# Performance work log

Hardware: AMD Instinct MI355X
Metric: run time of the kernel (lower is better)

## Reference

```python
import jax, jax.numpy as jnp
import numpy as np

B, T, IN, H = 4096, 128, 768, 256


def setup_inputs() -> dict:
    key = jax.random.key(0)
    ks = jax.random.split(key, 5)
    s1 = 1.0 / np.sqrt(IN)
    s2 = 1.0 / np.sqrt(H)
    return {
        "x": jax.random.normal(ks[0], (B, IN), jnp.float32),
        "W1": jax.random.normal(ks[1], (T, IN, H), jnp.float32) * s1,
        "b1": jnp.zeros((T, H), jnp.float32),
        "W2": jax.random.normal(ks[2], (T, H, H), jnp.float32) * s2,
        "b2": jnp.zeros((T, H), jnp.float32),
        "W3": jax.random.normal(ks[3], (T, H), jnp.float32) * s2,
        "b3": jnp.zeros((T,), jnp.float32),
    }


def reference(x, W1, b1, W2, b2, W3, b3):
    # Per-task 3-layer MLP, vectorized over tasks. Dropout is eval-mode (identity).
    h = jax.nn.relu(jnp.einsum('bi,tih->bth', x, W1) + b1)          # [B, T, H]
    h = jax.nn.relu(jnp.einsum('bth,thk->btk', h, W2) + b2)         # [B, T, H]
    out = jnp.einsum('bth,th->bt', h, W3) + b3                      # [B, T]
    return out
```

## Files before the change

### kernel.cpp

```cpp
#include <hip/hip_runtime.h>
#include <cstdint>
#include <cstddef>

#define B_   4096
#define T_   128
#define IN_  768
#define H_   256
#define BM_  128
#define KC1  (IN_ / 32)
#define NS1  48
#define NS2  16

typedef __bf16 bf16_t;
typedef bf16_t bf16x8 __attribute__((ext_vector_type(8)));
typedef bf16_t bf16x4 __attribute__((ext_vector_type(4)));
typedef float  floatx16 __attribute__((ext_vector_type(16)));

#define MFMA32(a, b, c) __builtin_amdgcn_mfma_f32_32x32x16_bf16((a), (b), (c), 0, 0, 0)

__device__ __forceinline__ void lgkm0_barrier() {
    asm volatile("s_waitcnt lgkmcnt(0)" ::: "memory");
    __builtin_amdgcn_s_barrier();
    asm volatile("" ::: "memory");
}

__global__ __launch_bounds__(256)
void tile_all(const float* __restrict__ x, const float* __restrict__ W1,
              const float* __restrict__ W2, bf16_t* __restrict__ xt,
              bf16_t* __restrict__ w1t, bf16_t* __restrict__ w2t) {
    const int b   = blockIdx.x;
    const int tid = threadIdx.x;
    if (b < T_ * KC1 + T_ * 8) {
        const float* src; bf16_t* dst; int t, kc, K, KC;
        if (b < T_ * KC1) { t = b / KC1; kc = b - t * KC1; K = IN_; KC = KC1; src = W1; dst = w1t; }
        else { int bb = b - T_ * KC1; t = bb >> 3; kc = bb & 7; K = H_; KC = 8; src = W2; dst = w2t; }
        const int kq = tid >> 6, h4 = (tid & 63) * 4;
        const float* s = src + ((size_t)t * K + kc * 32 + kq * 8) * H_ + h4;
        float r[8][4];
#pragma unroll
        for (int e = 0; e < 8; ++e) {
            float4 v = *(const float4*)(s + (size_t)e * H_);
            r[e][0] = v.x; r[e][1] = v.y; r[e][2] = v.z; r[e][3] = v.w;
        }
        bf16_t* d = dst + (((size_t)(t * KC + kc) * 4 + kq) * H_ + h4) * 8;
#pragma unroll
        for (int c = 0; c < 4; ++c) {
            bf16x8 v;
#pragma unroll
            for (int e = 0; e < 8; ++e) v[e] = (bf16_t)r[e][c];
            *(bf16x8*)(d + c * 8) = v;
        }
    } else {
        const int bb = b - (T_ * KC1 + T_ * 8);
        const int mb = bb / KC1, kc = bb - mb * KC1;
        const int r = tid >> 3, c = tid & 7;
#pragma unroll
        for (int it = 0; it < 4; ++it) {
            const int m = it * 32 + r;
            float4 v = *(const float4*)(x + ((size_t)(mb * 128 + m)) * IN_ + kc * 32 + c * 4);
            bf16x4 o; o[0] = (bf16_t)v.x; o[1] = (bf16_t)v.y; o[2] = (bf16_t)v.z; o[3] = (bf16_t)v.w;
            *(bf16x4*)(xt + ((size_t)(mb * KC1 + kc) * 4 + (c >> 1)) * 1024 + m * 8 + (c & 1) * 4) = o;
        }
    }
}

__global__ __launch_bounds__(256, 2)
void mtmlp_fused6(const bf16_t* __restrict__ xt, const bf16_t* __restrict__ w1t,
                  const float* __restrict__ b1, const bf16_t* __restrict__ w2t,
                  const float* __restrict__ b2, const float* __restrict__ W3,
                  const float* __restrict__ b3, float* __restrict__ out) {
    const int L    = blockIdx.x;
    const int xcd  = L & 7;
    const int idx  = L >> 3;
    const int t    = xcd * 16 + (idx >> 5);
    const int mblk = idx & 31;
    const int m0   = mblk * BM_;

    const int tid  = threadIdx.x;
    const int lane = tid & 63;
    const int wid  = tid >> 6;
    const int wm   = wid & 1;
    const int wn   = wid >> 1;
    const int ln31 = lane & 31;
    const int hi   = lane >> 5;

    __shared__ __align__(16) bf16_t hbuf[BM_ * H_];
    __shared__ __align__(16) bf16_t wring[2 * 4096];
    float* w3s = (float*)wring;

    floatx16 acc[2][2];
#pragma unroll
    for (int i = 0; i < 2; ++i)
#pragma unroll
        for (int j = 0; j < 2; ++j)
#pragma unroll
            for (int e = 0; e < 16; ++e) acc[i][j][e] = 0.0f;
    floatx16 acc2[2][2];
#pragma unroll
    for (int i = 0; i < 2; ++i)
#pragma unroll
        for (int j = 0; j < 2; ++j)
#pragma unroll
            for (int e = 0; e < 16; ++e) acc2[i][j][e] = 0.0f;

    const bf16_t* w1base = w1t + (size_t)t * NS1 * 4096;
    const bf16_t* w2base = w2t + (size_t)t * NS2 * 4096;
    const bf16_t* xbase  = xt + (size_t)mblk * KC1 * 4096;
    const int woff = tid * 16;
    const int xoff = (wn * 64 + ln31) * 8;

    bf16x8 wrA[2], wrB[2], xcur[2], xnxt[2];

    auto loadW = [&](bf16x8* r, const bf16_t* base, int c) {
        const bf16_t* p = base + (size_t)c * 4096 + woff;
        r[0] = *(const bf16x8*)(p);
        r[1] = *(const bf16x8*)(p + 8);
    };
    auto writeW = [&](const bf16x8* r, int sl) {
        bf16_t* p = wring + sl * 4096 + woff;
        *(bf16x8*)(p)     = r[0];
        *(bf16x8*)(p + 8) = r[1];
    };
    auto loadX = [&](bf16x8* r, int c) {
        const bf16_t* p = xbase + ((size_t)((c >> 1) * 4 + (c & 1) * 2 + hi)) * 1024 + xoff;
        r[0] = *(const bf16x8*)(p);
        r[1] = *(const bf16x8*)(p + 256);
    };
    auto comp = [&](const bf16x8* xf, int sl) {
        const bf16_t* buf = wring + sl * 4096;
        bf16x8 A0 = *(const bf16x8*)(buf + (size_t)(hi * 256 + wm * 128 + 0 * 32 + ln31) * 8);
        bf16x8 A1 = *(const bf16x8*)(buf + (size_t)(hi * 256 + wm * 128 + 1 * 32 + ln31) * 8);
        bf16x8 A2 = *(const bf16x8*)(buf + (size_t)(hi * 256 + wm * 128 + 2 * 32 + ln31) * 8);
        bf16x8 A3 = *(const bf16x8*)(buf + (size_t)(hi * 256 + wm * 128 + 3 * 32 + ln31) * 8);
#pragma unroll
        for (int j = 0; j < 2; ++j) {
            acc[0][j]  = MFMA32(A0, xf[j], acc[0][j]);
            acc[1][j]  = MFMA32(A1, xf[j], acc[1][j]);
            acc2[0][j] = MFMA32(A2, xf[j], acc2[0][j]);
            acc2[1][j] = MFMA32(A3, xf[j], acc2[1][j]);
        }
    };

    loadW(wrA, w1base, 0); loadW(wrB, w1base, 1); loadX(xcur, 0);
    writeW(wrA, 0);
    lgkm0_barrier();

    for (int c = 0; c < NS1 - 2; c += 2) {
        writeW(wrB, 1);
        loadW(wrA, w1base, c + 2);
        loadX(xnxt, c + 1);
        comp(xcur, 0);
        lgkm0_barrier();
        writeW(wrA, 0);
        loadW(wrB, w1base, c + 3);
        loadX(xcur, c + 2);
        comp(xnxt, 1);
        lgkm0_barrier();
    }
    writeW(wrB, 1);
    loadX(xnxt, 47);
    loadW(wrA, w2base, 0);
    loadW(wrB, w2base, 1);
    comp(xcur, 0);
    lgkm0_barrier();
    comp(xnxt, 1);

    {
        const floatx16* accp[4] = {&acc[0][0], nullptr, nullptr, nullptr};
#pragma unroll
        for (int i = 0; i < 4; ++i) {
            const floatx16* a0 = (i < 2) ? &acc[i][0] : &acc2[i - 2][0];
#pragma unroll
            for (int g = 0; g < 4; ++g) {
                const int h0 = wm * 128 + i * 32 + g * 8 + 4 * hi;
                float4 bias = *(const float4*)(b1 + t * H_ + h0);
                const int blk = h0 >> 3;
#pragma unroll
                for (int j = 0; j < 2; ++j) {
                    const int mm = wn * 64 + j * 32 + ln31;
                    const floatx16& a = a0[j];
                    bf16x4 o;
                    o[0] = (bf16_t)fmaxf(a[4 * g + 0] + bias.x, 0.0f);
                    o[1] = (bf16_t)fmaxf(a[4 * g + 1] + bias.y, 0.0f);
                    o[2] = (bf16_t)fmaxf(a[4 * g + 2] + bias.z, 0.0f);
                    o[3] = (bf16_t)fmaxf(a[4 * g + 3] + bias.w, 0.0f);
                    *(bf16x4*)(hbuf + (size_t)(blk * BM_ + mm) * 8 + 4 * hi) = o;
                }
            }
        }
        (void)accp;
    }
#pragma unroll
    for (int i = 0; i < 2; ++i)
#pragma unroll
        for (int j = 0; j < 2; ++j)
#pragma unroll
            for (int e = 0; e < 16; ++e) { acc[i][j][e] = 0.0f; acc2[i][j][e] = 0.0f; }

    writeW(wrA, 0);
    lgkm0_barrier();

    auto comp2 = [&](int c, int sl) {
        bf16x8 Bf[2];
        const int blk = c * 2 + hi;
#pragma unroll
        for (int j = 0; j < 2; ++j) {
            const int mm = wn * 64 + j * 32 + ln31;
            Bf[j] = *(const bf16x8*)(hbuf + (size_t)(blk * BM_ + mm) * 8);
        }
        comp(Bf, sl);
    };

    for (int c = 0; c < NS2 - 2; c += 2) {
        writeW(wrB, 1);
        loadW(wrA, w2base, c + 2);
        comp2(c, 0);
        lgkm0_barrier();
        writeW(wrA, 0);
        loadW(wrB, w2base, c + 3);
        comp2(c + 1, 1);
        lgkm0_barrier();
    }
    writeW(wrB, 1);
    comp2(14, 0);
    lgkm0_barrier();
    if (tid < H_) w3s[tid] = W3[t * H_ + tid];
    comp2(15, 1);
    lgkm0_barrier();

#pragma unroll
    for (int i = 0; i < 4; ++i) {
        const floatx16* a0 = (i < 2) ? &acc[i][0] : &acc2[i - 2][0];
#pragma unroll
        for (int g = 0; g < 4; ++g) {
            const int h0 = wm * 128 + i * 32 + g * 8 + 4 * hi;
            float4 bias = *(const float4*)(b2 + t * H_ + h0);
            const int blk = h0 >> 3;
#pragma unroll
            for (int j = 0; j < 2; ++j) {
                const int mm = wn * 64 + j * 32 + ln31;
                const floatx16& a = a0[j];
                bf16x4 o;
                o[0] = (bf16_t)fmaxf(a[4 * g + 0] + bias.x, 0.0f);
                o[1] = (bf16_t)fmaxf(a[4 * g + 1] + bias.y, 0.0f);
                o[2] = (bf16_t)fmaxf(a[4 * g + 2] + bias.z, 0.0f);
                o[3] = (bf16_t)fmaxf(a[4 * g + 3] + bias.w, 0.0f);
                *(bf16x4*)(hbuf + (size_t)(blk * BM_ + mm) * 8 + 4 * hi) = o;
            }
        }
    }
    lgkm0_barrier();

    {
        const int m = tid >> 1, seg = tid & 1;
        float sum = 0.0f;
#pragma unroll
        for (int b = 0; b < 16; ++b) {
            const int blk = seg * 16 + b;
            const bf16x8 v = *(const bf16x8*)(hbuf + (size_t)(blk * BM_ + m) * 8);
            const float* w = w3s + blk * 8;
#pragma unroll
            for (int e = 0; e < 8; ++e) sum += (float)v[e] * w[e];
        }
        sum += __shfl_xor(sum, 1);
        if (seg == 0) out[(size_t)(m0 + m) * T_ + t] = sum + b3[t];
    }
}

extern "C" void kernel_launch(void* const* d_in, const int* in_sizes, int n_in,
                              void* d_out, int out_size, void* d_ws, size_t ws_size,
                              hipStream_t stream) {
    const float* x  = (const float*)d_in[0];
    const float* W1 = (const float*)d_in[1];
    const float* b1 = (const float*)d_in[2];
    const float* W2 = (const float*)d_in[3];
    const float* b2 = (const float*)d_in[4];
    const float* W3 = (const float*)d_in[5];
    const float* b3 = (const float*)d_in[6];
    float* out = (float*)d_out;

    const size_t nx  = (size_t)B_ * IN_;
    const size_t nw1 = (size_t)T_ * IN_ * H_;

    bf16_t* xt  = (bf16_t*)d_ws;
    bf16_t* w1t = xt + nx;
    bf16_t* w2t = w1t + nw1;

    tile_all<<<dim3(T_ * KC1 + T_ * 8 + 32 * KC1), 256, 0, stream>>>(x, W1, W2, xt, w1t, w2t);
    mtmlp_fused6<<<dim3(4096), 256, 0, stream>>>(xt, w1t, b1, w2t, b2, W3, b3, out);
}
```

Baseline: 474.8 us.

## Remap blocks to batch tiles per XCD and stage x tiles through LDS

Changes the block-to-work mapping so each XCD handles a fixed set of 4 batch row-blocks across all tasks, instead of 16 tasks across all row-blocks. This keeps a small x working set per XCD L2 and streams the weights instead. In the first GEMM the x fragments are now loaded cooperatively into the hbuf LDS region and read from there, rather than each wave loading them directly from global memory. The weight copy into LDS is also reorganised into two strided 16-byte chunks per thread. The cost is an extra LDS write and read of x in every stage, plus a different L2 reuse pattern for the weights, which are now re-read by every XCD.

```diff
diff --git a/kernel.cpp b/kernel.cpp
--- a/kernel.cpp
+++ b/kernel.cpp
@@ -65,15 +65,15 @@
 }
 
 __global__ __launch_bounds__(256, 2)
-void mtmlp_fused6(const bf16_t* __restrict__ xt, const bf16_t* __restrict__ w1t,
+void mtmlp_fused7(const bf16_t* __restrict__ xt, const bf16_t* __restrict__ w1t,
                   const float* __restrict__ b1, const bf16_t* __restrict__ w2t,
                   const float* __restrict__ b2, const float* __restrict__ W3,
                   const float* __restrict__ b3, float* __restrict__ out) {
     const int L    = blockIdx.x;
     const int xcd  = L & 7;
-    const int idx  = L >> 3;
-    const int t    = xcd * 16 + (idx >> 5);
-    const int mblk = idx & 31;
+    const int s    = L >> 3;
+    const int t    = s >> 2;
+    const int mblk = xcd * 4 + (s & 3);
     const int m0   = mblk * BM_;
 
     const int tid  = threadIdx.x;
@@ -88,107 +88,101 @@
     __shared__ __align__(16) bf16_t wring[2 * 4096];
     float* w3s = (float*)wring;
 
-    floatx16 acc[2][2];
+    floatx16 acc[2][2], acc2[2][2];
 #pragma unroll
     for (int i = 0; i < 2; ++i)
 #pragma unroll
         for (int j = 0; j < 2; ++j)
 #pragma unroll
-            for (int e = 0; e < 16; ++e) acc[i][j][e] = 0.0f;
-    floatx16 acc2[2][2];
-#pragma unroll
-    for (int i = 0; i < 2; ++i)
-#pragma unroll
-        for (int j = 0; j < 2; ++j)
-#pragma unroll
-            for (int e = 0; e < 16; ++e) acc2[i][j][e] = 0.0f;
+            for (int e = 0; e < 16; ++e) { acc[i][j][e] = 0.0f; acc2[i][j][e] = 0.0f; }
 
     const bf16_t* w1base = w1t + (size_t)t * NS1 * 4096;
     const bf16_t* w2base = w2t + (size_t)t * NS2 * 4096;
     const bf16_t* xbase  = xt + (size_t)mblk * KC1 * 4096;
-    const int woff = tid * 16;
-    const int xoff = (wn * 64 + ln31) * 8;
-
-    bf16x8 wrA[2], wrB[2], xcur[2], xnxt[2];
+
+    bf16x8 wrA[2], wrB[2], xrA, xrB;
 
     auto loadW = [&](bf16x8* r, const bf16_t* base, int c) {
-        const bf16_t* p = base + (size_t)c * 4096 + woff;
+        const bf16_t* p = base + (size_t)c * 4096 + tid * 8;
         r[0] = *(const bf16x8*)(p);
-        r[1] = *(const bf16x8*)(p + 8);
+        r[1] = *(const bf16x8*)(p + 2048);
     };
     auto writeW = [&](const bf16x8* r, int sl) {
-        bf16_t* p = wring + sl * 4096 + woff;
-        *(bf16x8*)(p)     = r[0];
-        *(bf16x8*)(p + 8) = r[1];
-    };
-    auto loadX = [&](bf16x8* r, int c) {
-        const bf16_t* p = xbase + ((size_t)((c >> 1) * 4 + (c & 1) * 2 + hi)) * 1024 + xoff;
-        r[0] = *(const bf16x8*)(p);
-        r[1] = *(const bf16x8*)(p + 256);
-    };
-    auto comp = [&](const bf16x8* xf, int sl) {
-        const bf16_t* buf = wring + sl * 4096;
-        bf16x8 A0 = *(const bf16x8*)(buf + (size_t)(hi * 256 + wm * 128 + 0 * 32 + ln31) * 8);
-        bf16x8 A1 = *(const bf16x8*)(buf + (size_t)(hi * 256 + wm * 128 + 1 * 32 + ln31) * 8);
-        bf16x8 A2 = *(const bf16x8*)(buf + (size_t)(hi * 256 + wm * 128 + 2 * 32 + ln31) * 8);
-        bf16x8 A3 = *(const bf16x8*)(buf + (size_t)(hi * 256 + wm * 128 + 3 * 32 + ln31) * 8);
+        bf16_t* p = wring + sl * 4096 + tid * 8;
+        *(bf16x8*)(p)        = r[0];
+        *(bf16x8*)(p + 2048) = r[1];
+    };
+    auto loadXg = [&](bf16x8& r, int c) {
+        r = *(const bf16x8*)(xbase + (size_t)c * 2048 + tid * 8);
+    };
+    auto writeX = [&](const bf16x8& r, int sl) {
+        *(bf16x8*)(hbuf + sl * 2048 + tid * 8) = r;
+    };
+    auto comp = [&](int wsl, int xsl) {
+        const bf16_t* wb = wring + wsl * 4096;
+        const bf16_t* xb = hbuf + xsl * 2048;
+        bf16x8 A0 = *(const bf16x8*)(wb + (size_t)(hi * 256 + wm * 128 + 0 * 32 + ln31) * 8);
+        bf16x8 A1 = *(const bf16x8*)(wb + (size_t)(hi * 256 + wm * 128 + 1 * 32 + ln31) * 8);
+        bf16x8 A2 = *(const bf16x8*)(wb + (size_t)(hi * 256 + wm * 128 + 2 * 32 + ln31) * 8);
+        bf16x8 A3 = *(const bf16x8*)(wb + (size_t)(hi * 256 + wm * 128 + 3 * 32 + ln31) * 8);
+        bf16x8 Bf[2];
+#pragma unroll
+        for (int j = 0; j < 2; ++j)
+            Bf[j] = *(const bf16x8*)(xb + (size_t)(hi * 128 + wn * 64 + j * 32 + ln31) * 8);
 #pragma unroll
         for (int j = 0; j < 2; ++j) {
-            acc[0][j]  = MFMA32(A0, xf[j], acc[0][j]);
-            acc[1][j]  = MFMA32(A1, xf[j], acc[1][j]);
-            acc2[0][j] = MFMA32(A2, xf[j], acc2[0][j]);
-            acc2[1][j] = MFMA32(A3, xf[j], acc2[1][j]);
-        }
-    };
-
-    loadW(wrA, w1base, 0); loadW(wrB, w1base, 1); loadX(xcur, 0);
-    writeW(wrA, 0);
+            acc[0][j]  = MFMA32(A0, Bf[j], acc[0][j]);
+            acc[1][j]  = MFMA32(A1, Bf[j], acc[1][j]);
+            acc2[0][j] = MFMA32(A2, Bf[j], acc2[0][j]);
+            acc2[1][j] = MFMA32(A3, Bf[j], acc2[1][j]);
+        }
+    };
+
+    loadW(wrA, w1base, 0); loadXg(xrA, 0);
+    loadW(wrB, w1base, 1); loadXg(xrB, 1);
+    writeW(wrA, 0); writeX(xrA, 0);
     lgkm0_barrier();
 
     for (int c = 0; c < NS1 - 2; c += 2) {
-        writeW(wrB, 1);
-        loadW(wrA, w1base, c + 2);
-        loadX(xnxt, c + 1);
-        comp(xcur, 0);
-        lgkm0_barrier();
-        writeW(wrA, 0);
-        loadW(wrB, w1base, c + 3);
-        loadX(xcur, c + 2);
-        comp(xnxt, 1);
-        lgkm0_barrier();
-    }
-    writeW(wrB, 1);
-    loadX(xnxt, 47);
+        writeW(wrB, 1); writeX(xrB, 1);
+        loadW(wrA, w1base, c + 2); loadXg(xrA, c + 2);
+        comp(0, 0);
+        lgkm0_barrier();
+        writeW(wrA, 0); writeX(xrA, 0);
+        loadW(wrB, w1base, c + 3); loadXg(xrB, c + 3);
+        comp(1, 1);
+        lgkm0_barrier();
+    }
+    writeW(wrB, 1); writeX(xrB, 1);
     loadW(wrA, w2base, 0);
     loadW(wrB, w2base, 1);
-    comp(xcur, 0);
-    lgkm0_barrier();
-    comp(xnxt, 1);
-
-    {
-        const floatx16* accp[4] = {&acc[0][0], nullptr, nullptr, nullptr};
-#pragma unroll
-        for (int i = 0; i < 4; ++i) {
-            const floatx16* a0 = (i < 2) ? &acc[i][0] : &acc2[i - 2][0];
-#pragma unroll
-            for (int g = 0; g < 4; ++g) {
-                const int h0 = wm * 128 + i * 32 + g * 8 + 4 * hi;
-                float4 bias = *(const float4*)(b1 + t * H_ + h0);
-                const int blk = h0 >> 3;
-#pragma unroll
-                for (int j = 0; j < 2; ++j) {
-                    const int mm = wn * 64 + j * 32 + ln31;
-                    const floatx16& a = a0[j];
-                    bf16x4 o;
-                    o[0] = (bf16_t)fmaxf(a[4 * g + 0] + bias.x, 0.0f);
-                    o[1] = (bf16_t)fmaxf(a[4 * g + 1] + bias.y, 0.0f);
-                    o[2] = (bf16_t)fmaxf(a[4 * g + 2] + bias.z, 0.0f);
-                    o[3] = (bf16_t)fmaxf(a[4 * g + 3] + bias.w, 0.0f);
-                    *(bf16x4*)(hbuf + (size_t)(blk * BM_ + mm) * 8 + 4 * hi) = o;
-                }
+    comp(0, 0);
+    lgkm0_barrier();
+    comp(1, 1);
+    lgkm0_barrier();
+
+    writeW(wrA, 0);
+
+#pragma unroll
+    for (int i = 0; i < 4; ++i) {
+        const floatx16* a0 = (i < 2) ? &acc[i][0] : &acc2[i - 2][0];
+#pragma unroll
+        for (int g = 0; g < 4; ++g) {
+            const int h0 = wm * 128 + i * 32 + g * 8 + 4 * hi;
+            float4 bias = *(const float4*)(b1 + t * H_ + h0);
+            const int blk = h0 >> 3;
+#pragma unroll
+            for (int j = 0; j < 2; ++j) {
+                const int mm = wn * 64 + j * 32 + ln31;
+                const floatx16& a = a0[j];
+                bf16x4 o;
+                o[0] = (bf16_t)fmaxf(a[4 * g + 0] + bias.x, 0.0f);
+                o[1] = (bf16_t)fmaxf(a[4 * g + 1] + bias.y, 0.0f);
+                o[2] = (bf16_t)fmaxf(a[4 * g + 2] + bias.z, 0.0f);
+                o[3] = (bf16_t)fmaxf(a[4 * g + 3] + bias.w, 0.0f);
+                *(bf16x4*)(hbuf + (size_t)(blk * BM_ + mm) * 8 + 4 * hi) = o;
             }
         }
-        (void)accp;
     }
 #pragma unroll
     for (int i = 0; i < 2; ++i)
@@ -197,10 +191,14 @@
 #pragma unroll
             for (int e = 0; e < 16; ++e) { acc[i][j][e] = 0.0f; acc2[i][j][e] = 0.0f; }
 
-    writeW(wrA, 0);
     lgkm0_barrier();
 
     auto comp2 = [&](int c, int sl) {
+        const bf16_t* wb = wring + sl * 4096;
+        bf16x8 A0 = *(const bf16x8*)(wb + (size_t)(hi * 256 + wm * 128 + 0 * 32 + ln31) * 8);
+        bf16x8 A1 = *(const bf16x8*)(wb + (size_t)(hi * 256 + wm * 128 + 1 * 32 + ln31) * 8);
+        bf16x8 A2 = *(const bf16x8*)(wb + (size_t)(hi * 256 + wm * 128 + 2 * 32 + ln31) * 8);
+        bf16x8 A3 = *(const bf16x8*)(wb + (size_t)(hi * 256 + wm * 128 + 3 * 32 + ln31) * 8);
         bf16x8 Bf[2];
         const int blk = c * 2 + hi;
 #pragma unroll
@@ -208,7 +206,13 @@
             const int mm = wn * 64 + j * 32 + ln31;
             Bf[j] = *(const bf16x8*)(hbuf + (size_t)(blk * BM_ + mm) * 8);
         }
-        comp(Bf, sl);
+#pragma unroll
+        for (int j = 0; j < 2; ++j) {
+            acc[0][j]  = MFMA32(A0, Bf[j], acc[0][j]);
+            acc[1][j]  = MFMA32(A1, Bf[j], acc[1][j]);
+            acc2[0][j] = MFMA32(A2, Bf[j], acc2[0][j]);
+            acc2[1][j] = MFMA32(A3, Bf[j], acc2[1][j]);
+        }
     };
 
     for (int c = 0; c < NS2 - 2; c += 2) {
@@ -224,7 +228,7 @@
     writeW(wrB, 1);
     comp2(14, 0);
     lgkm0_barrier();
-    if (tid < H_) w3s[tid] = W3[t * H_ + tid];
+    w3s[tid] = W3[t * H_ + tid];
     comp2(15, 1);
     lgkm0_barrier();
 
@@ -287,5 +291,5 @@
     bf16_t* w2t = w1t + nw1;
 
     tile_all<<<dim3(T_ * KC1 + T_ * 8 + 32 * KC1), 256, 0, stream>>>(x, W1, W2, xt, w1t, w2t);
-    mtmlp_fused6<<<dim3(4096), 256, 0, stream>>>(xt, w1t, b1, w2t, b2, W3, b3, out);
-}
+    mtmlp_fused7<<<dim3(4096), 256, 0, stream>>>(xt, w1t, b1, w2t, b2, W3, b3, out);
+}
```

After: 484.2 us. Within noise of the previous version (+2.0%).
